# Optimization experiments

Measured on AMD Instinct MI355X. Metric: run time of the kernel, lower is better.

The kernel has to match this reference:

```python
import math
import jax, jax.numpy as jnp
import numpy as np

# ---------------- static structure (mirrors CG_woFilter_cuda + MyBatchNormWeightMM) ----------------
LMAX = 4
TAUS = [16, 16, 16, 16, 16]          # t_F: input channels per degree l
T_O  = [16, 16, 16, 16, 16]          # output channels per degree l after weight matmul
BN_EPS = 1e-5

# all (l, l1, l2) triples with l2 <= l1 <= lmax and |l1-l2| <= l <= min(l1+l2, lmax), sorted by (l,l1,l2)
TRIPLES = sorted([(l, l1, l2)
                  for l1 in range(LMAX + 1)
                  for l2 in range(l1 + 1)
                  for l in range(l1 - l2, min(l1 + l2, LMAX) + 1)])

T_FF = [0] * (LMAX + 1)              # t_FF[l] = sum over triples of taus[l1]*taus[l2]
for (l, l1, l2) in TRIPLES:
    T_FF[l] += TAUS[l1] * TAUS[l2]

def _cg_coef(j1, m1, j2, m2, j, m):
    """Clebsch-Gordan coefficient <j1 m1 j2 m2 | j m> (Condon-Shortley)."""
    if m1 + m2 != m:
        return 0.0
    f = math.factorial
    if j < abs(j1 - j2) or j > j1 + j2:
        return 0.0
    pref = math.sqrt((2 * j + 1) * f(j + j1 - j2) * f(j - j1 + j2) * f(j1 + j2 - j) / f(j1 + j2 + j + 1))
    pref *= math.sqrt(f(j + m) * f(j - m) * f(j1 - m1) * f(j1 + m1) * f(j2 - m2) * f(j2 + m2))
    s = 0.0
    for k in range(0, j1 + j2 - j + 1):
        if (j1 - m1 - k) < 0 or (j2 + m2 - k) < 0 or (j - j2 + m1 + k) < 0 or (j - j1 - m2 + k) < 0:
            continue
        s += ((-1.0) ** k) / (f(k) * f(j1 + j2 - j - k) * f(j1 - m1 - k)
                              * f(j2 + m2 - k) * f(j - j2 + m1 + k) * f(j - j1 - m2 + k))
    return pref * s

def _cg_matrix(l, l1, l2):
    C = np.zeros((2 * l + 1, 2 * l1 + 1, 2 * l2 + 1), dtype=np.float32)
    for m in range(-l, l + 1):
        for m1 in range(-l1, l1 + 1):
            m2 = m - m1
            if -l2 <= m2 <= l2:
                C[m + l, m1 + l1, m2 + l2] = _cg_coef(l1, m1, l2, m2, l, m)
    return C

CG_MATS = {t: jnp.asarray(_cg_matrix(*t)) for t in TRIPLES}

M_IN = sum(TAUS[l] * (2 * l + 1) for l in range(LMAX + 1))      # 400
W_LEN = sum(T_FF[l] * T_O[l] for l in range(LMAX + 1))          # 172032


def setup_inputs() -> dict:
    key = jax.random.key(0)
    k1, k2 = jax.random.split(key)
    B = 256
    Fs = jax.random.normal(k1, (B, M_IN, 2), dtype=jnp.float32)
    W = jax.random.normal(k2, (W_LEN, 2), dtype=jnp.float32) * 0.05
    return {"Fs": Fs, "W": W}


def reference(Fs, W):
    B = Fs.shape[0]
    # split input into per-degree blocks: F_l [B, tau, 2l+1, 2]
    Fl, off = [], 0
    for l in range(LMAX + 1):
        n = TAUS[l] * (2 * l + 1)
        Fl.append(Fs[:, off:off + n, :].reshape(B, TAUS[l], 2 * l + 1, 2))
        off += n
    # sparse CG tensor product: per-triple complex outer product contracted with CG coefs
    frags = [[] for _ in range(LMAX + 1)]
    for (l, l1, l2) in TRIPLES:
        C = CG_MATS[(l, l1, l2)]                     # [2l+1, 2l1+1, 2l2+1]
        a, b = Fl[l1], Fl[l2]
        ar, ai = a[..., 0], a[..., 1]
        br, bi = b[..., 0], b[..., 1]
        rr = jnp.einsum('bip,bjq,mpq->bijm', ar, br, C)
        ii = jnp.einsum('bip,bjq,mpq->bijm', ai, bi, C)
        ri = jnp.einsum('bip,bjq,mpq->bijm', ar, bi, C)
        ir = jnp.einsum('bip,bjq,mpq->bijm', ai, br, C)
        fr = (rr - ii).reshape(B, -1, 2 * l + 1)     # channels flattened as c1*tau2 + c2 (t_offsets order)
        fi = (ri + ir).reshape(B, -1, 2 * l + 1)
        frags[l].append(jnp.stack([fr, fi], axis=-1))
    # per-degree fragment batchnorm + complex weight matmul (FN_WMM)
    outs, woff = [], 0
    for l in range(LMAX + 1):
        FF = jnp.concatenate(frags[l], axis=1)       # [B, t_FF, 2l+1, 2]
        var = jnp.mean(jnp.sum(FF * FF, axis=-1), axis=(0, 2))      # per-channel mean |z|^2
        FFn = FF / (jnp.sqrt(var)[None, :, None, None] + BN_EPS)
        n = T_FF[l] * T_O[l]
        Wl = W[woff:woff + n].reshape(T_O[l], T_FF[l], 2)
        woff += n
        wr, wi = Wl[..., 0], Wl[..., 1]
        xr, xi = FFn[..., 0], FFn[..., 1]
        yr = jnp.einsum('oc,bcm->bom', wr, xr) - jnp.einsum('oc,bcm->bom', wi, xi)
        yi = jnp.einsum('oc,bcm->bom', wr, xi) + jnp.einsum('oc,bcm->bom', wi, xr)
        outs.append(jnp.stack([yr, yi], axis=-1).reshape(B, T_O[l] * (2 * l + 1), 2))
    return jnp.concatenate(outs, axis=1)             # [B, sum t_O[l]*(2l+1), 2] = [B, 400, 2]
```

## Files before the change

kernel.cpp:

```cpp
#include <hip/hip_runtime.h>
#include <math.h>

#define NTRI 42
#define NCH  10752
#define B_SZ 256
#define AH_PL 172032

typedef float    f32x4 __attribute__((ext_vector_type(4)));
typedef _Float16 half8 __attribute__((ext_vector_type(8)));
typedef _Float16 f16x2 __attribute__((ext_vector_type(2)));

constexpr int CT_L [NTRI]={0,0,0,0,0, 1,1,1,1,1,1,1,1, 2,2,2,2,2,2,2,2,2,2, 3,3,3,3,3,3,3,3,3,3, 4,4,4,4,4,4,4,4,4};
constexpr int CT_L1[NTRI]={0,1,2,3,4, 1,1,2,2,3,3,4,4, 1,2,2,2,3,3,3,4,4,4, 2,2,3,3,3,3,4,4,4,4, 2,3,3,3,4,4,4,4,4};
constexpr int CT_L2[NTRI]={0,1,2,3,4, 0,1,1,2,2,3,3,4, 1,0,1,2,1,2,3,2,3,4, 1,2,0,1,2,3,1,2,3,4, 2,1,2,3,0,1,2,3,4};
constexpr int CT_T [NTRI]={0,1,2,3,4, 0,1,2,3,4,5,6,7, 0,1,2,3,4,5,6,7,8,9, 0,1,2,3,4,5,6,7,8,9, 0,1,2,3,4,5,6,7,8};

constexpr int KL_t[5]    ={1280,2048,2560,2560,2304};
constexpr int GBASE_t[5] ={0,1280,3328,5888,8448};
constexpr int ROFF_t[5]  ={0,16,64,144,256};
constexpr int FFB_t[5]   ={0,327680,1900544,5177344,9764864};
#define FF_TOT 15073280
constexpr int PL_t[5]    ={0,5,29,79,149};
#define PART_PL 4096
#define PART_TOT (230*PART_PL)

__device__ const int   dCTL[NTRI]={0,0,0,0,0, 1,1,1,1,1,1,1,1, 2,2,2,2,2,2,2,2,2,2, 3,3,3,3,3,3,3,3,3,3, 4,4,4,4,4,4,4,4,4};
__device__ const int   dCTT[NTRI]={0,1,2,3,4, 0,1,2,3,4,5,6,7, 0,1,2,3,4,5,6,7,8,9, 0,1,2,3,4,5,6,7,8,9, 0,1,2,3,4,5,6,7,8};
__device__ const int   dK[5]   ={1280,2048,2560,2560,2304};
__device__ const int   dWOFF[5]={0,20480,53248,94208,135168};
__device__ const int   dNM[5]  ={1,3,5,7,9};
__device__ const int   dFFB[5] ={0,327680,1900544,5177344,9764864};
__device__ const int   dPL[5]  ={0,5,29,79,149};
__device__ const int   dGB[5]  ={0,1280,3328,5888,8448};
__device__ const int   dROFF[5]={0,16,64,144,256};
__device__ const int   dNT[5]  ={5,8,10,10,9};
__device__ const float dINV[5] ={1.f/256.f,1.f/768.f,1.f/1280.f,1.f/1792.f,1.f/2304.f};

__device__ float  g_vpart[64*NCH];
__device__ __align__(16) f16x2  g_ff[FF_TOT];
__device__ __align__(16) f16x2  g_ah[2*AH_PL];
__device__ float2 g_part[PART_TOT];

constexpr double cfact(int n){ double r=1.0; for(int i=2;i<=n;i++) r*=(double)i; return r; }
constexpr double csqrt_(double v){ double x = v>1.0? v:1.0; for(int i=0;i<80;i++) x = 0.5*(x+v/x); return x; }
constexpr double ccg(int j1,int m1,int j2,int m2,int j,int m){
    if(m1+m2!=m) return 0.0;
    double pref = csqrt_((2.0*j+1.0)*cfact(j+j1-j2)*cfact(j-j1+j2)*cfact(j1+j2-j)/cfact(j1+j2+j+1));
    pref *= csqrt_(cfact(j+m)*cfact(j-m)*cfact(j1-m1)*cfact(j1+m1)*cfact(j2-m2)*cfact(j2+m2));
    double s=0.0;
    for(int k=0;k<=j1+j2-j;k++){
        int a=j1-m1-k, bb=j2+m2-k, c=j-j2+m1+k, d=j-j1-m2+k;
        if(a<0||bb<0||c<0||d<0) continue;
        double term = 1.0/(cfact(k)*cfact(j1+j2-j-k)*cfact(a)*cfact(bb)*cfact(c)*cfact(d));
        s += (k&1)? -term : term;
    }
    return pref*s;
}
struct CG81 { float a[81]; };
constexpr CG81 makecg(int l,int l1,int l2){
    CG81 t{};
    const int n1=2*l1+1;
    for(int mi=0;mi<2*l+1;mi++)
        for(int p=0;p<n1;p++){
            const int m=mi-l, m1=p-l1, m2=m-m1;
            if(m2>=-l2 && m2<=l2) t.a[mi*n1+p]=(float)ccg(l1,m1,l2,m2,l,m);
        }
    return t;
}
template<int TR> struct CGC { static constexpr CG81 t = makecg(CT_L[TR],CT_L1[TR],CT_L2[TR]); };

template<int TR>
__device__ __forceinline__ void cg_compute(const float2* __restrict__ FsB,
                                           int i, int j, float2* __restrict__ ff){
    constexpr int L=CT_L[TR], L1=CT_L1[TR], L2=CT_L2[TR];
    constexpr int N1=2*L1+1, N2=2*L2+1, NM=2*L+1;
    float2 A[N1], Bv[N2];
    #pragma unroll
    for(int p=0;p<N1;p++) A[p]=FsB[ROFF_t[L1]+i*N1+p];
    #pragma unroll
    for(int q=0;q<N2;q++) Bv[q]=FsB[ROFF_t[L2]+j*N2+q];
    #pragma unroll
    for(int mi=0;mi<NM;mi++){
        float aR=0.f, aI=0.f;
        const int pLo = (mi-L+L1-L2) > 0 ? (mi-L+L1-L2) : 0;
        const int pHi = (mi-L+L1+L2) < 2*L1 ? (mi-L+L1+L2) : 2*L1;
        #pragma unroll
        for(int p=0;p<N1;p++){
            if(p>=pLo && p<=pHi){
                const float c = CGC<TR>::t.a[mi*N1+p];
                if(c != 0.f){
                    const int q = mi - L - p + L1 + L2;
                    const float2 a=A[p], b=Bv[q];
                    aR = fmaf(c, a.x*b.x - a.y*b.y, aR);
                    aI = fmaf(c, a.x*b.y + a.y*b.x, aI);
                }
            }
        }
        ff[mi]=make_float2(aR,aI);
    }
}

template<int TR>
__device__ __forceinline__ void cg_one(const float2* __restrict__ Fs, int bc, int t){
    constexpr int L=CT_L[TR], NM=2*L+1, T=CT_T[TR], K=KL_t[L];
    constexpr int MPL=256*K;
    const int i=t>>4, j=t&15;
    float n2=0.f;
    for(int b4=0;b4<4;b4++){
        const int b=bc*4+b4;
        float2 ff[NM];
        cg_compute<TR>(Fs + b*400, i, j, ff);
        const int base = FFB_t[L] + b*K + T*256 + t;
        #pragma unroll
        for(int m=0;m<NM;m++){
            n2 = fmaf(ff[m].x,ff[m].x,n2);
            n2 = fmaf(ff[m].y,ff[m].y,n2);
            f16x2 h; h.x=(_Float16)ff[m].x; h.y=(_Float16)ff[m].y;
            g_ff[base + m*MPL] = h;
        }
    }
    g_vpart[bc*NCH + GBASE_t[L] + CT_T[TR]*256 + t] = n2;
}

template<int TR>
__device__ __forceinline__ void cg_disp(int tr, const float2* Fs, int bc, int t){
    if constexpr (TR < NTRI){
        if(tr==TR) cg_one<TR>(Fs,bc,t);
        else       cg_disp<TR+1>(tr,Fs,bc,t);
    }
}

__global__ void __launch_bounds__(256) k_cg(const float2* __restrict__ Fs){
    cg_disp<0>(blockIdx.x, Fs, blockIdx.y, threadIdx.x);
}

__global__ void __launch_bounds__(256) k_wn(const float2* __restrict__ W2){
    const int tr=blockIdx.x, t=threadIdx.x;
    const int l=dCTL[tr], T=dCTT[tr], K=dK[l];
    const int ch = dGB[l] + T*256 + t;
    float s=0.f;
    #pragma unroll 8
    for(int bc=0;bc<64;bc++) s += g_vpart[bc*NCH + ch];
    const float invv = 1.f/(sqrtf(s*dINV[l])+1e-5f);
    const int base = dWOFF[l] + T*256 + t;
    #pragma unroll 4
    for(int o=0;o<16;o++){
        const float2 w = W2[base + o*K];
        f16x2 hr, hi;
        hr.x=(_Float16)( w.x*invv); hr.y=(_Float16)(-w.y*invv);
        hi.x=(_Float16)( w.y*invv); hi.y=(_Float16)( w.x*invv);
        g_ah[base + o*K]         = hr;
        g_ah[AH_PL + base + o*K] = hi;
    }
}

__global__ void __launch_bounds__(256) k_mm(){
    const int j=blockIdx.x;
    const int wv=threadIdx.x>>6, lane=threadIdx.x&63;
    const int bg=blockIdx.y*4+wv;
    const int l=(j<5)?0:(j<29)?1:(j<79)?2:(j<149)?3:4;
    const int nm=dNM[l];
    const int loc=j-dPL[l];
    const int T=loc/nm, m=loc-T*nm;
    const int K=dK[l];
    const int l15=lane&15, kg=lane>>4;
    const half8* __restrict__ Arp = reinterpret_cast<const half8*>(g_ah + dWOFF[l] + l15*K + T*256 + kg*4);
    const half8* __restrict__ Aip = reinterpret_cast<const half8*>(g_ah + AH_PL + dWOFF[l] + l15*K + T*256 + kg*4);
    const half8* __restrict__ Xp  = reinterpret_cast<const half8*>(g_ff + dFFB[l] + m*(K<<8) + (bg*16+l15)*K + T*256 + kg*4);
    f32x4 ar0={0.f,0.f,0.f,0.f}, ar1={0.f,0.f,0.f,0.f};
    f32x4 ai0={0.f,0.f,0.f,0.f}, ai1={0.f,0.f,0.f,0.f};
    #pragma unroll
    for(int ks=0; ks<16; ks++){
        const half8 Ar = Arp[ks*4];
        const half8 Ai = Aip[ks*4];
        const half8 Bf = Xp [ks*4];
        if(ks & 1){
            ar1 = __builtin_amdgcn_mfma_f32_16x16x32_f16(Ar, Bf, ar1, 0,0,0);
            ai1 = __builtin_amdgcn_mfma_f32_16x16x32_f16(Ai, Bf, ai1, 0,0,0);
        } else {
            ar0 = __builtin_amdgcn_mfma_f32_16x16x32_f16(Ar, Bf, ar0, 0,0,0);
            ai0 = __builtin_amdgcn_mfma_f32_16x16x32_f16(Ai, Bf, ai0, 0,0,0);
        }
    }
    const f32x4 ar = ar0 + ar1, ai = ai0 + ai1;
    float2* __restrict__ pp = g_part + j*PART_PL + bg*256;
    #pragma unroll
    for(int r=0;r<4;r++){
        pp[(kg*4+r)*16 + l15] = make_float2(ar[r], ai[r]);
    }
}

__global__ void __launch_bounds__(448) k_red(float2* __restrict__ out){
    const int b=blockIdx.x, r=threadIdx.x;
    if(r>=400) return;
    const int l = (r<16)?0:(r<64)?1:(r<144)?2:(r<256)?3:4;
    const int om = r - dROFF[l];
    const int nm = dNM[l];
    const int o = om/nm, m = om - o*nm;
    const float2* __restrict__ pp = g_part + (dPL[l]+m)*PART_PL + (b>>4)*256 + o*16 + (b&15);
    float2 s=make_float2(0.f,0.f);
    const int nt=dNT[l];
    for(int T=0;T<nt;T++){
        const float2 v = pp[T*nm*PART_PL];
        s.x+=v.x; s.y+=v.y;
    }
    out[b*400+r]=s;
}

extern "C" void kernel_launch(void* const* d_in, const int* in_sizes, int n_in,
                              void* d_out, int out_size, void* d_ws, size_t ws_size,
                              hipStream_t stream){
    const float2* Fs = (const float2*)d_in[0];
    const float2* W  = (const float2*)d_in[1];
    float2* out = (float2*)d_out;

    k_cg <<<dim3(NTRI,64), 256, 0, stream>>>(Fs);
    k_wn <<<dim3(NTRI),    256, 0, stream>>>(W);
    k_mm <<<dim3(230,4),   256, 0, stream>>>();
    k_red<<<dim3(B_SZ),    448, 0, stream>>>(out);
}
```

Baseline: 121.3 us.

## Split CG kernel to one batch per block and stage inputs in LDS

The CG fragment kernel now launches one block per (triple, batch element) instead of looping over four batch elements per block. Each block first stages that batch element's 400 complex inputs into shared memory with vectorized loads, then reads them from LDS. The per-channel variance partials grow from 64 to 256 rows, so the weight-normalization kernel must sum four times as many entries in its single small grid. This raises parallelism in the CG stage but adds work to the serial reduction in k_wn.

Result: slower. 139.8 us (+15.3%).

```diff
diff --git a/kernel.cpp b/kernel.cpp
--- a/kernel.cpp
+++ b/kernel.cpp
@@ -36,7 +36,7 @@
 __device__ const int   dNT[5]  ={5,8,10,10,9};
 __device__ const float dINV[5] ={1.f/256.f,1.f/768.f,1.f/1280.f,1.f/1792.f,1.f/2304.f};
 
-__device__ float  g_vpart[64*NCH];
+__device__ float  g_vpart[B_SZ*NCH];
 __device__ __align__(16) f16x2  g_ff[FF_TOT];
 __device__ __align__(16) f16x2  g_ah[2*AH_PL];
 __device__ float2 g_part[PART_TOT];
@@ -70,15 +70,15 @@
 template<int TR> struct CGC { static constexpr CG81 t = makecg(CT_L[TR],CT_L1[TR],CT_L2[TR]); };
 
 template<int TR>
-__device__ __forceinline__ void cg_compute(const float2* __restrict__ FsB,
-                                           int i, int j, float2* __restrict__ ff){
+__device__ __forceinline__ void cg_compute_lds(const float2* __restrict__ sF,
+                                               int i, int j, float2* __restrict__ ff){
     constexpr int L=CT_L[TR], L1=CT_L1[TR], L2=CT_L2[TR];
     constexpr int N1=2*L1+1, N2=2*L2+1, NM=2*L+1;
     float2 A[N1], Bv[N2];
     #pragma unroll
-    for(int p=0;p<N1;p++) A[p]=FsB[ROFF_t[L1]+i*N1+p];
-    #pragma unroll
-    for(int q=0;q<N2;q++) Bv[q]=FsB[ROFF_t[L2]+j*N2+q];
+    for(int p=0;p<N1;p++) A[p]=sF[ROFF_t[L1]+i*N1+p];
+    #pragma unroll
+    for(int q=0;q<N2;q++) Bv[q]=sF[ROFF_t[L2]+j*N2+q];
     #pragma unroll
     for(int mi=0;mi<NM;mi++){
         float aR=0.f, aI=0.f;
@@ -101,37 +101,39 @@
 }
 
 template<int TR>
-__device__ __forceinline__ void cg_one(const float2* __restrict__ Fs, int bc, int t){
+__device__ __forceinline__ void cg_one(const float2* __restrict__ sF, int b, int t){
     constexpr int L=CT_L[TR], NM=2*L+1, T=CT_T[TR], K=KL_t[L];
     constexpr int MPL=256*K;
     const int i=t>>4, j=t&15;
+    float2 ff[NM];
+    cg_compute_lds<TR>(sF, i, j, ff);
     float n2=0.f;
-    for(int b4=0;b4<4;b4++){
-        const int b=bc*4+b4;
-        float2 ff[NM];
-        cg_compute<TR>(Fs + b*400, i, j, ff);
-        const int base = FFB_t[L] + b*K + T*256 + t;
-        #pragma unroll
-        for(int m=0;m<NM;m++){
-            n2 = fmaf(ff[m].x,ff[m].x,n2);
-            n2 = fmaf(ff[m].y,ff[m].y,n2);
-            f16x2 h; h.x=(_Float16)ff[m].x; h.y=(_Float16)ff[m].y;
-            g_ff[base + m*MPL] = h;
-        }
-    }
-    g_vpart[bc*NCH + GBASE_t[L] + CT_T[TR]*256 + t] = n2;
+    const int base = FFB_t[L] + b*K + T*256 + t;
+    #pragma unroll
+    for(int m=0;m<NM;m++){
+        n2 = fmaf(ff[m].x,ff[m].x,n2);
+        n2 = fmaf(ff[m].y,ff[m].y,n2);
+        f16x2 h; h.x=(_Float16)ff[m].x; h.y=(_Float16)ff[m].y;
+        g_ff[base + m*MPL] = h;
+    }
+    g_vpart[b*NCH + GBASE_t[L] + T*256 + t] = n2;
 }
 
 template<int TR>
-__device__ __forceinline__ void cg_disp(int tr, const float2* Fs, int bc, int t){
+__device__ __forceinline__ void cg_disp(int tr, const float2* sF, int b, int t){
     if constexpr (TR < NTRI){
-        if(tr==TR) cg_one<TR>(Fs,bc,t);
-        else       cg_disp<TR+1>(tr,Fs,bc,t);
+        if(tr==TR) cg_one<TR>(sF,b,t);
+        else       cg_disp<TR+1>(tr,sF,b,t);
     }
 }
 
 __global__ void __launch_bounds__(256) k_cg(const float2* __restrict__ Fs){
-    cg_disp<0>(blockIdx.x, Fs, blockIdx.y, threadIdx.x);
+    __shared__ float2 sF[400];
+    const int b=blockIdx.y, t=threadIdx.x;
+    const float4* __restrict__ F4 = reinterpret_cast<const float4*>(Fs) + b*200;
+    if(t<200) reinterpret_cast<float4*>(sF)[t] = F4[t];
+    __syncthreads();
+    cg_disp<0>(blockIdx.x, sF, b, t);
 }
 
 __global__ void __launch_bounds__(256) k_wn(const float2* __restrict__ W2){
@@ -140,7 +142,7 @@
     const int ch = dGB[l] + T*256 + t;
     float s=0.f;
     #pragma unroll 8
-    for(int bc=0;bc<64;bc++) s += g_vpart[bc*NCH + ch];
+    for(int b=0;b<256;b++) s += g_vpart[b*NCH + ch];
     const float invv = 1.f/(sqrtf(s*dINV[l])+1e-5f);
     const int base = dWOFF[l] + T*256 + t;
     #pragma unroll 4
@@ -214,8 +216,8 @@
     const float2* W  = (const float2*)d_in[1];
     float2* out = (float2*)d_out;
 
-    k_cg <<<dim3(NTRI,64), 256, 0, stream>>>(Fs);
-    k_wn <<<dim3(NTRI),    256, 0, stream>>>(W);
-    k_mm <<<dim3(230,4),   256, 0, stream>>>();
-    k_red<<<dim3(B_SZ),    448, 0, stream>>>(out);
-}
+    k_cg <<<dim3(NTRI,B_SZ), 256, 0, stream>>>(Fs);
+    k_wn <<<dim3(NTRI),      256, 0, stream>>>(W);
+    k_mm <<<dim3(230,4),     256, 0, stream>>>();
+    k_red<<<dim3(B_SZ),      448, 0, stream>>>(out);
+}
```

## Stage Fs rows in LDS for CG kernel and interleave fragment layout by batch

Applied to the files above, without the earlier changes.

The CG kernel now copies the four batch rows of Fs it needs into shared memory once per block, then reads the A and B vectors from LDS rather than global memory. The fragment buffer layout changes from [m][b][K] to [b][m][K], so each batch's 2l+1 components are contiguous. The matmul kernel's X pointer is updated to match. The batch loop is also unrolled. This cuts redundant global loads and improves locality of the fragment writes, at the cost of a block-wide sync and 12.8 KB of LDS per block.

Measured after the change: 120.8 us. No clear change (-0.4%).

```diff
diff --git a/kernel.cpp b/kernel.cpp
--- a/kernel.cpp
+++ b/kernel.cpp
@@ -18,6 +18,7 @@
 constexpr int KL_t[5]    ={1280,2048,2560,2560,2304};
 constexpr int GBASE_t[5] ={0,1280,3328,5888,8448};
 constexpr int ROFF_t[5]  ={0,16,64,144,256};
+constexpr int NM_t[5]    ={1,3,5,7,9};
 constexpr int FFB_t[5]   ={0,327680,1900544,5177344,9764864};
 #define FF_TOT 15073280
 constexpr int PL_t[5]    ={0,5,29,79,149};
@@ -70,15 +71,15 @@
 template<int TR> struct CGC { static constexpr CG81 t = makecg(CT_L[TR],CT_L1[TR],CT_L2[TR]); };
 
 template<int TR>
-__device__ __forceinline__ void cg_compute(const float2* __restrict__ FsB,
-                                           int i, int j, float2* __restrict__ ff){
+__device__ __forceinline__ void cg_compute_lds(const float2* __restrict__ sF,
+                                               int i, int j, float2* __restrict__ ff){
     constexpr int L=CT_L[TR], L1=CT_L1[TR], L2=CT_L2[TR];
     constexpr int N1=2*L1+1, N2=2*L2+1, NM=2*L+1;
     float2 A[N1], Bv[N2];
     #pragma unroll
-    for(int p=0;p<N1;p++) A[p]=FsB[ROFF_t[L1]+i*N1+p];
-    #pragma unroll
-    for(int q=0;q<N2;q++) Bv[q]=FsB[ROFF_t[L2]+j*N2+q];
+    for(int p=0;p<N1;p++) A[p]=sF[ROFF_t[L1]+i*N1+p];
+    #pragma unroll
+    for(int q=0;q<N2;q++) Bv[q]=sF[ROFF_t[L2]+j*N2+q];
     #pragma unroll
     for(int mi=0;mi<NM;mi++){
         float aR=0.f, aI=0.f;
@@ -101,37 +102,46 @@
 }
 
 template<int TR>
-__device__ __forceinline__ void cg_one(const float2* __restrict__ Fs, int bc, int t){
+__device__ __forceinline__ void cg_one(const float2* __restrict__ sF, int bc, int t){
     constexpr int L=CT_L[TR], NM=2*L+1, T=CT_T[TR], K=KL_t[L];
-    constexpr int MPL=256*K;
+    constexpr int NMK=NM*K;
     const int i=t>>4, j=t&15;
     float n2=0.f;
+    #pragma unroll
     for(int b4=0;b4<4;b4++){
         const int b=bc*4+b4;
         float2 ff[NM];
-        cg_compute<TR>(Fs + b*400, i, j, ff);
-        const int base = FFB_t[L] + b*K + T*256 + t;
+        cg_compute_lds<TR>(sF + b4*400, i, j, ff);
+        const int base = FFB_t[L] + b*NMK + T*256 + t;
         #pragma unroll
         for(int m=0;m<NM;m++){
             n2 = fmaf(ff[m].x,ff[m].x,n2);
             n2 = fmaf(ff[m].y,ff[m].y,n2);
             f16x2 h; h.x=(_Float16)ff[m].x; h.y=(_Float16)ff[m].y;
-            g_ff[base + m*MPL] = h;
-        }
-    }
-    g_vpart[bc*NCH + GBASE_t[L] + CT_T[TR]*256 + t] = n2;
+            g_ff[base + m*K] = h;
+        }
+    }
+    g_vpart[bc*NCH + GBASE_t[L] + T*256 + t] = n2;
 }
 
 template<int TR>
-__device__ __forceinline__ void cg_disp(int tr, const float2* Fs, int bc, int t){
+__device__ __forceinline__ void cg_disp(int tr, const float2* sF, int bc, int t){
     if constexpr (TR < NTRI){
-        if(tr==TR) cg_one<TR>(Fs,bc,t);
-        else       cg_disp<TR+1>(tr,Fs,bc,t);
+        if(tr==TR) cg_one<TR>(sF,bc,t);
+        else       cg_disp<TR+1>(tr,sF,bc,t);
     }
 }
 
 __global__ void __launch_bounds__(256) k_cg(const float2* __restrict__ Fs){
-    cg_disp<0>(blockIdx.x, Fs, blockIdx.y, threadIdx.x);
+    __shared__ float4 sF4[800];
+    const int bc=blockIdx.y, t=threadIdx.x;
+    const float4* __restrict__ F4 = reinterpret_cast<const float4*>(Fs) + bc*800;
+    sF4[t]      = F4[t];
+    sF4[t+256]  = F4[t+256];
+    sF4[t+512]  = F4[t+512];
+    if(t<32) sF4[t+768] = F4[t+768];
+    __syncthreads();
+    cg_disp<0>(blockIdx.x, reinterpret_cast<const float2*>(sF4), bc, t);
 }
 
 __global__ void __launch_bounds__(256) k_wn(const float2* __restrict__ W2){
@@ -166,7 +176,7 @@
     const int l15=lane&15, kg=lane>>4;
     const half8* __restrict__ Arp = reinterpret_cast<const half8*>(g_ah + dWOFF[l] + l15*K + T*256 + kg*4);
     const half8* __restrict__ Aip = reinterpret_cast<const half8*>(g_ah + AH_PL + dWOFF[l] + l15*K + T*256 + kg*4);
-    const half8* __restrict__ Xp  = reinterpret_cast<const half8*>(g_ff + dFFB[l] + m*(K<<8) + (bg*16+l15)*K + T*256 + kg*4);
+    const half8* __restrict__ Xp  = reinterpret_cast<const half8*>(g_ff + dFFB[l] + (bg*16+l15)*(nm*K) + m*K + T*256 + kg*4);
     f32x4 ar0={0.f,0.f,0.f,0.f}, ar1={0.f,0.f,0.f,0.f};
     f32x4 ai0={0.f,0.f,0.f,0.f}, ai1={0.f,0.f,0.f,0.f};
     #pragma unroll
```
